# Performance work log

Measured on AMD Instinct MI355X. Metric: run time of the kernel, lower is better.

## Reference

```python
import jax, jax.numpy as jnp
import numpy as np

DIM = 192
HEADS = 6
WIN = (2, 7, 7)
N = WIN[0] * WIN[1] * WIN[2]  # 98
B_ = 2048
NW = 512


def _relative_position_index():
    d, h, w = np.meshgrid(np.arange(WIN[0]), np.arange(WIN[1]), np.arange(WIN[2]), indexing='ij')
    coords = np.stack([d.ravel(), h.ravel(), w.ravel()])  # [3, N]
    rel = coords[:, :, None] - coords[:, None, :]          # [3, N, N]
    rel = rel.transpose(1, 2, 0).astype(np.int64)
    rel[:, :, 0] += WIN[0] - 1
    rel[:, :, 1] += WIN[1] - 1
    rel[:, :, 2] += WIN[2] - 1
    rel[:, :, 0] *= (2 * WIN[1] - 1) * (2 * WIN[2] - 1)
    rel[:, :, 1] *= 2 * WIN[2] - 1
    return rel.sum(-1).astype(np.int32)  # [N, N]


def setup_inputs() -> dict:
    key = jax.random.key(0)
    ks = jax.random.split(key, 6)
    table_size = (2 * WIN[0] - 1) * (2 * WIN[1] - 1) * (2 * WIN[2] - 1)  # 507
    return {
        'x': jax.random.normal(ks[0], (B_, N, DIM), dtype=jnp.float32),
        'mask': jnp.zeros((NW, N, N), dtype=jnp.float32),
        'qkv_w': jax.random.normal(ks[1], (3 * DIM, DIM), dtype=jnp.float32) * 0.02,
        'qkv_b': jnp.zeros((3 * DIM,), dtype=jnp.float32),
        'proj_w': jax.random.normal(ks[2], (DIM, DIM), dtype=jnp.float32) * 0.02,
        'proj_b': jnp.zeros((DIM,), dtype=jnp.float32),
        'bias_table': jax.random.truncated_normal(ks[3], -2.0, 2.0, (table_size, HEADS), dtype=jnp.float32) * 0.02,
        'rel_idx': jnp.asarray(_relative_position_index()),
    }


def reference(x, mask, qkv_w, qkv_b, proj_w, proj_b, bias_table, rel_idx):
    b_, n, c = x.shape
    hd = c // HEADS
    scale = hd ** -0.5
    qkv = x @ qkv_w.T + qkv_b                      # [B_, N, 3C]
    qkv = qkv.reshape(b_, n, 3, HEADS, hd).transpose(2, 0, 3, 1, 4)
    q, k, v = qkv[0], qkv[1], qkv[2]               # each [B_, H, N, hd]
    attn = jnp.einsum('bhnd,bhmd->bhnm', q * scale, k)
    # relative position bias gather: [N*N] -> [N, N, H] -> [H, N, N]
    bias = bias_table[rel_idx.reshape(-1)].reshape(n, n, HEADS).transpose(2, 0, 1)
    attn = attn + bias[None]
    nw = mask.shape[0]
    attn = attn.reshape(b_ // nw, nw, HEADS, n, n) + mask[None, :, None]
    attn = attn.reshape(b_, HEADS, n, n)
    attn = jax.nn.softmax(attn, axis=-1)
    out = jnp.einsum('bhnm,bhmd->bhnd', attn, v)   # [B_, H, N, hd]
    out = out.transpose(0, 2, 1, 3).reshape(b_, n, c)
    return out @ proj_w.T + proj_b
```

## Files before the change

### kernel.cpp

```cpp
#include <hip/hip_runtime.h>
#include <hip/hip_bf16.h>
#include <stdint.h>

#define SEQ    98
#define DIMC   192
#define NHEADS 6
#define HDIM   32
#define NBATCH 2048
#define NWIN   512
#define SCALE  0.17677669529663687f

#define OFF_QKVW  0u
#define OFF_PROJW 221184u
#define OFF_BIAS  294912u
#define OFF_FLAGS 445440u
#define OFF_Q     447488u
#define PERWIN_E  (NHEADS * SEQ * HDIM)
#define PERWIN_B  ((size_t)PERWIN_E * 2 * 3)

typedef __attribute__((ext_vector_type(4)))  float f32x4;
typedef __attribute__((ext_vector_type(16))) float f32x16;
typedef __attribute__((ext_vector_type(8)))  short bf16x8;

static __device__ __forceinline__ uint16_t f2bf(float f) {
    uint32_t u = __builtin_bit_cast(uint32_t, f);
    u += 0x7fffu + ((u >> 16) & 1u);
    return (uint16_t)(u >> 16);
}
static __device__ __forceinline__ float bf2f(uint16_t h) {
    uint32_t u = ((uint32_t)h) << 16;
    return __builtin_bit_cast(float, u);
}

__global__ void __launch_bounds__(256) k_prep(
    const float* __restrict__ qkv_w, const float* __restrict__ proj_w,
    const float* __restrict__ bias_table, const int* __restrict__ rel_idx,
    uint16_t* __restrict__ qkv_wb, uint16_t* __restrict__ proj_wb,
    uint16_t* __restrict__ bias6b)
{
    int idx = blockIdx.x * 256 + threadIdx.x;
    if (idx < 110592) {
        qkv_wb[idx] = f2bf(qkv_w[idx]);
    } else if (idx < 147456) {
        int t = idx - 110592;
        proj_wb[t] = f2bf(proj_w[t]);
    } else {
        int t = idx - 147456;
        int h = t / (112 * 112);
        int rr = t % (112 * 112);
        int i = rr / 112, j = rr % 112;
        float v = -1e30f;
        if (i < SEQ && j < SEQ) v = bias_table[rel_idx[i * SEQ + j] * NHEADS + h];
        bias6b[t] = f2bf(v);
    }
}

__global__ void __launch_bounds__(256) k_flags(const float* __restrict__ mask,
                                               int* __restrict__ flags)
{
    int w = blockIdx.x;
    __shared__ int sf;
    if (threadIdx.x == 0) sf = 0;
    __syncthreads();
    const float* m = mask + (size_t)w * (SEQ * SEQ);
    int local = 0;
    for (int i = threadIdx.x; i < SEQ * SEQ; i += 256) local |= (m[i] != 0.0f);
    if (local) atomicOr(&sf, 1);
    __syncthreads();
    if (threadIdx.x == 0) flags[w] = sf;
}

__global__ void __launch_bounds__(256) k_qkv(
    const float* __restrict__ x, const float* __restrict__ qkv_b,
    const uint16_t* __restrict__ qkv_wb,
    uint16_t* __restrict__ q_ws, uint16_t* __restrict__ k_ws,
    uint16_t* __restrict__ v_ws, int b0)
{
    __shared__ uint16_t xs[128][200];
    const int lb = blockIdx.x, b = b0 + lb, tid = threadIdx.x;
    const int lane = tid & 63, wave = tid >> 6;
    const int l31 = lane & 31, lh = lane >> 5;

    const float4* x4 = (const float4*)(x + (size_t)b * SEQ * DIMC);
    for (int i = tid; i < SEQ * DIMC / 4; i += 256) {
        float4 v = x4[i];
        int row = i / 48, col = (i % 48) * 4;
        union { uint16_t s[4]; uint2 u; } pk;
        pk.s[0] = f2bf(v.x); pk.s[1] = f2bf(v.y);
        pk.s[2] = f2bf(v.z); pk.s[3] = f2bf(v.w);
        *(uint2*)&xs[row][col] = pk.u;
    }
    for (int i = tid; i < 30 * 100; i += 256) {
        int row = 98 + i / 100, c2 = (i % 100) * 2;
        *(uint32_t*)&xs[row][c2] = 0;
    }
    __syncthreads();

    for (int mt = 0; mt < 4; mt++) {
        bf16x8 afr[12];
        #pragma unroll
        for (int kk = 0; kk < 12; kk++)
            afr[kk] = *(const bf16x8*)&xs[mt * 32 + l31][kk * 16 + lh * 8];

        for (int ot = wave; ot < 18; ot += 4) {
            const uint16_t* wp = qkv_wb + (size_t)(ot * 32 + l31) * DIMC + lh * 8;
            bf16x8 bfr[12];
            #pragma unroll
            for (int kk = 0; kk < 12; kk++)
                bfr[kk] = *(const bf16x8*)(wp + kk * 16);
            float qb = qkv_b[ot * 32 + l31];

            f32x16 acc;
            #pragma unroll
            for (int i = 0; i < 16; i++) acc[i] = 0.0f;
            #pragma unroll
            for (int kk = 0; kk < 12; kk++)
                acc = __builtin_amdgcn_mfma_f32_32x32x16_bf16(afr[kk], bfr[kk], acc, 0, 0, 0);

            const int sec = ot / 6, head = ot % 6;
            uint16_t* outp = (sec == 0 ? q_ws : sec == 1 ? k_ws : v_ws)
                           + (size_t)(lb * NHEADS + head) * SEQ * HDIM + l31;
            #pragma unroll
            for (int r = 0; r < 16; r++) {
                int row = mt * 32 + 4 * lh + (r & 3) + 8 * (r >> 2);
                if (row < SEQ) outp[row * HDIM] = f2bf(acc[r] + qb);
            }
        }
    }
}

__global__ void __launch_bounds__(256) k_attn(
    const uint16_t* __restrict__ q_ws, const uint16_t* __restrict__ k_ws,
    const uint16_t* __restrict__ v_ws, const uint16_t* __restrict__ bias6b,
    const float* __restrict__ mask, const int* __restrict__ flags,
    const uint16_t* __restrict__ proj_wb, const float* __restrict__ proj_b,
    float* __restrict__ out, int b0)
{
    __shared__ uint16_t att_s[98][200];
    __shared__ uint16_t k_s[98][40];
    __shared__ uint16_t vT_s[32][136];
    __shared__ uint16_t p_s[4][16][40];

    const int lb = blockIdx.x, b = b0 + lb, tid = threadIdx.x;
    const int lane = tid & 63, wave = tid >> 6;
    const int l15 = lane & 15, lq = lane >> 4;
    const int useMask = flags[b & (NWIN - 1)];
    const float* maskp = mask + (size_t)(b & (NWIN - 1)) * (SEQ * SEQ);

    for (int i = tid; i < 32 * 20; i += 256) {
        int row = i / 20, c = 96 + (i % 20) * 2;
        *(uint32_t*)&vT_s[row][c] = 0;
    }

    for (int h = 0; h < NHEADS; h++) {
        if (h) __syncthreads();
        const uint32_t* kp = (const uint32_t*)(k_ws + (size_t)(lb * NHEADS + h) * SEQ * HDIM);
        const uint32_t* vp = (const uint32_t*)(v_ws + (size_t)(lb * NHEADS + h) * SEQ * HDIM);
        for (int i = tid; i < SEQ * 16; i += 256) {
            int row = i >> 4, cp = i & 15;
            uint32_t kv = kp[i];
            *(uint32_t*)&k_s[row][cp * 2] = kv;
            uint32_t vv = vp[i];
            vT_s[cp * 2][row]     = (uint16_t)(vv & 0xffff);
            vT_s[cp * 2 + 1][row] = (uint16_t)(vv >> 16);
        }
        __syncthreads();

        for (int mt = wave; mt < 7; mt += 4) {
            int qrow = mt * 16 + l15; qrow = qrow < SEQ ? qrow : SEQ - 1;
            bf16x8 aq = *(const bf16x8*)(q_ws +
                ((size_t)(lb * NHEADS + h) * SEQ + qrow) * HDIM + lq * 8);

            f32x4 sacc[7];
            #pragma unroll
            for (int jt = 0; jt < 7; jt++) {
                int krow = jt * 16 + l15; krow = krow < SEQ ? krow : SEQ - 1;
                bf16x8 bk = *(const bf16x8*)&k_s[krow][lq * 8];
                f32x4 z = {0.f, 0.f, 0.f, 0.f};
                sacc[jt] = __builtin_amdgcn_mfma_f32_16x16x32_bf16(aq, bk, z, 0, 0, 0);
            }

            float p[7][4], rowmax[4], rowsum[4];
            #pragma unroll
            for (int r = 0; r < 4; r++) rowmax[r] = -3e38f;
            #pragma unroll
            for (int jt = 0; jt < 7; jt++) {
                int j = jt * 16 + l15;
                #pragma unroll
                for (int r = 0; r < 4; r++) {
                    int i_ = mt * 16 + lq * 4 + r;
                    float s = sacc[jt][r] * SCALE +
                              bf2f(bias6b[(h * 112 + i_) * 112 + j]);
                    if (useMask && i_ < SEQ && j < SEQ) s += maskp[i_ * SEQ + j];
                    p[jt][r] = s;
                    rowmax[r] = fmaxf(rowmax[r], s);
                }
            }
            #pragma unroll
            for (int r = 0; r < 4; r++) {
                float m = rowmax[r];
                m = fmaxf(m, __shfl_xor(m, 1));
                m = fmaxf(m, __shfl_xor(m, 2));
                m = fmaxf(m, __shfl_xor(m, 4));
                m = fmaxf(m, __shfl_xor(m, 8));
                rowmax[r] = m; rowsum[r] = 0.f;
            }
            #pragma unroll
            for (int jt = 0; jt < 7; jt++)
                #pragma unroll
                for (int r = 0; r < 4; r++) {
                    float e = __expf(p[jt][r] - rowmax[r]);
                    p[jt][r] = e; rowsum[r] += e;
                }
            #pragma unroll
            for (int r = 0; r < 4; r++) {
                float s2 = rowsum[r];
                s2 += __shfl_xor(s2, 1);
                s2 += __shfl_xor(s2, 2);
                s2 += __shfl_xor(s2, 4);
                s2 += __shfl_xor(s2, 8);
                rowsum[r] = 1.0f / s2;
            }

            f32x4 oacc[2];
            oacc[0] = (f32x4){0.f,0.f,0.f,0.f};
            oacc[1] = (f32x4){0.f,0.f,0.f,0.f};
            #pragma unroll
            for (int kk = 0; kk < 4; kk++) {
                int t1 = kk * 2 + 1;
                #pragma unroll
                for (int r = 0; r < 4; r++) {
                    p_s[wave][lq * 4 + r][l15]      = f2bf(p[kk * 2][r]);
                    p_s[wave][lq * 4 + r][16 + l15] = f2bf(t1 < 7 ? p[t1][r] : 0.f);
                }
                bf16x8 ap = *(const bf16x8*)&p_s[wave][l15][lq * 8];
                #pragma unroll
                for (int o = 0; o < 2; o++) {
                    bf16x8 bv = *(const bf16x8*)&vT_s[o * 16 + l15][kk * 32 + lq * 8];
                    oacc[o] = __builtin_amdgcn_mfma_f32_16x16x32_bf16(ap, bv, oacc[o], 0, 0, 0);
                }
            }
            #pragma unroll
            for (int o = 0; o < 2; o++)
                #pragma unroll
                for (int r = 0; r < 4; r++) {
                    int row = mt * 16 + lq * 4 + r;
                    if (row < SEQ)
                        att_s[row][h * HDIM + o * 16 + l15] =
                            f2bf(oacc[o][r] * rowsum[r]);
                }
        }
    }
    __syncthreads();

    for (int ot = wave; ot < 12; ot += 4) {
        const uint16_t* wp = proj_wb + (size_t)(ot * 16 + l15) * DIMC + lq * 8;
        bf16x8 bw[6];
        #pragma unroll
        for (int kk = 0; kk < 6; kk++) bw[kk] = *(const bf16x8*)(wp + kk * 32);
        float pb = proj_b[ot * 16 + l15];
        for (int mt = 0; mt < 7; mt++) {
            int arow = mt * 16 + l15; arow = arow < SEQ ? arow : SEQ - 1;
            f32x4 pacc = {0.f, 0.f, 0.f, 0.f};
            #pragma unroll
            for (int kk = 0; kk < 6; kk++) {
                bf16x8 aa = *(const bf16x8*)&att_s[arow][kk * 32 + lq * 8];
                pacc = __builtin_amdgcn_mfma_f32_16x16x32_bf16(aa, bw[kk], pacc, 0, 0, 0);
            }
            #pragma unroll
            for (int r = 0; r < 4; r++) {
                int row = mt * 16 + lq * 4 + r;
                if (row < SEQ)
                    out[((size_t)b * SEQ + row) * DIMC + ot * 16 + l15] = pacc[r] + pb;
            }
        }
    }
}

extern "C" void kernel_launch(void* const* d_in, const int* in_sizes, int n_in,
                              void* d_out, int out_size, void* d_ws, size_t ws_size,
                              hipStream_t stream) {
    const float* x          = (const float*)d_in[0];
    const float* mask       = (const float*)d_in[1];
    const float* qkv_w      = (const float*)d_in[2];
    const float* qkv_b      = (const float*)d_in[3];
    const float* proj_w     = (const float*)d_in[4];
    const float* proj_b     = (const float*)d_in[5];
    const float* bias_table = (const float*)d_in[6];
    const int*   rel_idx    = (const int*)d_in[7];
    float* out = (float*)d_out;
    char*  ws  = (char*)d_ws;

    uint16_t* qkv_wb  = (uint16_t*)(ws + OFF_QKVW);
    uint16_t* proj_wb = (uint16_t*)(ws + OFF_PROJW);
    uint16_t* bias6b  = (uint16_t*)(ws + OFF_BIAS);
    int*      flags   = (int*)(ws + OFF_FLAGS);

    int chunk = NBATCH;
    if (ws_size < (size_t)OFF_Q + (size_t)NBATCH * PERWIN_B) {
        size_t cap = ws_size > OFF_Q ? (ws_size - OFF_Q) / PERWIN_B : 1;
        if (cap < 1) cap = 1;
        if (cap > NBATCH) cap = NBATCH;
        chunk = (int)cap;
    }
    uint16_t* q_ws = (uint16_t*)(ws + OFF_Q);
    uint16_t* k_ws = q_ws + (size_t)chunk * PERWIN_E;
    uint16_t* v_ws = k_ws + (size_t)chunk * PERWIN_E;

    k_prep<<<870, 256, 0, stream>>>(qkv_w, proj_w, bias_table, rel_idx,
                                    qkv_wb, proj_wb, bias6b);
    k_flags<<<NWIN, 256, 0, stream>>>(mask, flags);
    for (int b0 = 0; b0 < NBATCH; b0 += chunk) {
        int nb = chunk < NBATCH - b0 ? chunk : NBATCH - b0;
        k_qkv<<<nb, 256, 0, stream>>>(x, qkv_b, qkv_wb, q_ws, k_ws, v_ws, b0);
        k_attn<<<nb, 256, 0, stream>>>(q_ws, k_ws, v_ws, bias6b, mask, flags,
                                       proj_wb, proj_b, out, b0);
    }
}
```

Before: 850.0 us.

## Split attention per head, move projection to separate GEMM kernel, vectorize stores

```diff
diff --git a/kernel.cpp b/kernel.cpp
--- a/kernel.cpp
+++ b/kernel.cpp
@@ -15,11 +15,10 @@
 #define OFF_BIAS  294912u
 #define OFF_FLAGS 445440u
 #define OFF_Q     447488u
-#define PERWIN_E  (NHEADS * SEQ * HDIM)
-#define PERWIN_B  ((size_t)PERWIN_E * 2 * 3)
+#define PERWIN_E  18816
+#define PERWIN_B  ((size_t)PERWIN_E * 2 * 4)
 
 typedef __attribute__((ext_vector_type(4)))  float f32x4;
-typedef __attribute__((ext_vector_type(16))) float f32x16;
 typedef __attribute__((ext_vector_type(8)))  short bf16x8;
 
 static __device__ __forceinline__ uint16_t f2bf(float f) {
@@ -30,6 +29,11 @@
 static __device__ __forceinline__ float bf2f(uint16_t h) {
     uint32_t u = ((uint32_t)h) << 16;
     return __builtin_bit_cast(float, u);
+}
+static __device__ __forceinline__ uint32_t cvtpk(float a, float b) {
+    uint32_t d;
+    asm("v_cvt_pk_bf16_f32 %0, %1, %2" : "=v"(d) : "v"(a), "v"(b));
+    return d;
 }
 
 __global__ void __launch_bounds__(256) k_prep(
@@ -70,209 +74,211 @@
     if (threadIdx.x == 0) flags[w] = sf;
 }
 
-__global__ void __launch_bounds__(256) k_qkv(
+__global__ void __launch_bounds__(256, 4) k_qkv(
     const float* __restrict__ x, const float* __restrict__ qkv_b,
     const uint16_t* __restrict__ qkv_wb,
     uint16_t* __restrict__ q_ws, uint16_t* __restrict__ k_ws,
     uint16_t* __restrict__ v_ws, int b0)
 {
-    __shared__ uint16_t xs[128][200];
+    __shared__ uint16_t xs[112][200];
+    __shared__ uint16_t obuf[4][16][40];
     const int lb = blockIdx.x, b = b0 + lb, tid = threadIdx.x;
     const int lane = tid & 63, wave = tid >> 6;
-    const int l31 = lane & 31, lh = lane >> 5;
+    const int l15 = lane & 15, lq = lane >> 4;
 
     const float4* x4 = (const float4*)(x + (size_t)b * SEQ * DIMC);
     for (int i = tid; i < SEQ * DIMC / 4; i += 256) {
         float4 v = x4[i];
         int row = i / 48, col = (i % 48) * 4;
-        union { uint16_t s[4]; uint2 u; } pk;
-        pk.s[0] = f2bf(v.x); pk.s[1] = f2bf(v.y);
-        pk.s[2] = f2bf(v.z); pk.s[3] = f2bf(v.w);
-        *(uint2*)&xs[row][col] = pk.u;
-    }
-    for (int i = tid; i < 30 * 100; i += 256) {
-        int row = 98 + i / 100, c2 = (i % 100) * 2;
-        *(uint32_t*)&xs[row][c2] = 0;
-    }
-    __syncthreads();
-
-    for (int mt = 0; mt < 4; mt++) {
-        bf16x8 afr[12];
-        #pragma unroll
-        for (int kk = 0; kk < 12; kk++)
-            afr[kk] = *(const bf16x8*)&xs[mt * 32 + l31][kk * 16 + lh * 8];
-
-        for (int ot = wave; ot < 18; ot += 4) {
-            const uint16_t* wp = qkv_wb + (size_t)(ot * 32 + l31) * DIMC + lh * 8;
-            bf16x8 bfr[12];
-            #pragma unroll
-            for (int kk = 0; kk < 12; kk++)
-                bfr[kk] = *(const bf16x8*)(wp + kk * 16);
-            float qb = qkv_b[ot * 32 + l31];
-
-            f32x16 acc;
-            #pragma unroll
-            for (int i = 0; i < 16; i++) acc[i] = 0.0f;
-            #pragma unroll
-            for (int kk = 0; kk < 12; kk++)
-                acc = __builtin_amdgcn_mfma_f32_32x32x16_bf16(afr[kk], bfr[kk], acc, 0, 0, 0);
-
-            const int sec = ot / 6, head = ot % 6;
-            uint16_t* outp = (sec == 0 ? q_ws : sec == 1 ? k_ws : v_ws)
-                           + (size_t)(lb * NHEADS + head) * SEQ * HDIM + l31;
-            #pragma unroll
-            for (int r = 0; r < 16; r++) {
-                int row = mt * 32 + 4 * lh + (r & 3) + 8 * (r >> 2);
-                if (row < SEQ) outp[row * HDIM] = f2bf(acc[r] + qb);
-            }
-        }
-    }
-}
-
-__global__ void __launch_bounds__(256) k_attn(
+        uint2 pk;
+        pk.x = cvtpk(v.x, v.y);
+        pk.y = cvtpk(v.z, v.w);
+        *(uint2*)&xs[row][col] = pk;
+    }
+    __syncthreads();
+
+    for (int ot = wave; ot < 18; ot += 4) {
+        bf16x8 bfr[2][6];
+        float qb[2];
+        #pragma unroll
+        for (int o = 0; o < 2; o++) {
+            const uint16_t* wp = qkv_wb + (size_t)(ot * 32 + o * 16 + l15) * DIMC + lq * 8;
+            #pragma unroll
+            for (int kk = 0; kk < 6; kk++) bfr[o][kk] = *(const bf16x8*)(wp + kk * 32);
+            qb[o] = qkv_b[ot * 32 + o * 16 + l15];
+        }
+        const int sec = ot / 6, head = ot % 6;
+        uint16_t* outp = (sec == 0 ? q_ws : sec == 1 ? k_ws : v_ws)
+                       + (size_t)(lb * NHEADS + head) * (SEQ * HDIM);
+        for (int mt = 0; mt < 7; mt++) {
+            bf16x8 afr[6];
+            #pragma unroll
+            for (int kk = 0; kk < 6; kk++)
+                afr[kk] = *(const bf16x8*)&xs[mt * 16 + l15][kk * 32 + lq * 8];
+            f32x4 a0 = {0.f,0.f,0.f,0.f}, a1 = {0.f,0.f,0.f,0.f};
+            #pragma unroll
+            for (int kk = 0; kk < 6; kk++) {
+                a0 = __builtin_amdgcn_mfma_f32_16x16x32_bf16(afr[kk], bfr[0][kk], a0, 0, 0, 0);
+                a1 = __builtin_amdgcn_mfma_f32_16x16x32_bf16(afr[kk], bfr[1][kk], a1, 0, 0, 0);
+            }
+            #pragma unroll
+            for (int r = 0; r < 4; r++) {
+                obuf[wave][lq * 4 + r][l15]      = f2bf(a0[r] + qb[0]);
+                obuf[wave][lq * 4 + r][16 + l15] = f2bf(a1[r] + qb[1]);
+            }
+            int r16 = lane >> 2, m8 = (lane & 3) * 8;
+            int token = mt * 16 + r16;
+            bf16x8 ov = *(const bf16x8*)&obuf[wave][r16][m8];
+            if (token < SEQ)
+                *(bf16x8*)(outp + token * HDIM + m8) = ov;
+        }
+    }
+}
+
+__global__ void __launch_bounds__(256, 4) k_attn(
     const uint16_t* __restrict__ q_ws, const uint16_t* __restrict__ k_ws,
     const uint16_t* __restrict__ v_ws, const uint16_t* __restrict__ bias6b,
     const float* __restrict__ mask, const int* __restrict__ flags,
-    const uint16_t* __restrict__ proj_wb, const float* __restrict__ proj_b,
-    float* __restrict__ out, int b0)
-{
-    __shared__ uint16_t att_s[98][200];
+    uint16_t* __restrict__ att, int b0)
+{
     __shared__ uint16_t k_s[98][40];
     __shared__ uint16_t vT_s[32][136];
-    __shared__ uint16_t p_s[4][16][40];
-
-    const int lb = blockIdx.x, b = b0 + lb, tid = threadIdx.x;
+    __shared__ uint16_t ps[4][16][40];
+
+    const int bid = blockIdx.x;
+    const int lb = bid / 6, h = bid % 6;
+    const int bg = b0 + lb;
+    const int tid = threadIdx.x, lane = tid & 63, wave = tid >> 6;
+    const int l15 = lane & 15, lq = lane >> 4;
+    const int useMask = flags[bg & (NWIN - 1)];
+    const float* maskp = mask + (size_t)(bg & (NWIN - 1)) * (SEQ * SEQ);
+
+    for (int i = tid; i < 32 * 19; i += 256) {
+        int d = i / 19, c = 98 + (i % 19) * 2;
+        *(uint32_t*)&vT_s[d][c] = 0;
+    }
+    const uint32_t* kp = (const uint32_t*)(k_ws + (size_t)(lb * NHEADS + h) * (SEQ * HDIM));
+    const uint32_t* vp = (const uint32_t*)(v_ws + (size_t)(lb * NHEADS + h) * (SEQ * HDIM));
+    for (int i = tid; i < SEQ * 16; i += 256) {
+        int row = i >> 4, cp = i & 15;
+        uint32_t kv = kp[i];
+        *(uint32_t*)&k_s[row][cp * 2] = kv;
+        uint32_t vv = vp[i];
+        vT_s[cp * 2][row]     = (uint16_t)(vv & 0xffff);
+        vT_s[cp * 2 + 1][row] = (uint16_t)(vv >> 16);
+    }
+    __syncthreads();
+
+    const uint16_t* qbase = q_ws + (size_t)(lb * NHEADS + h) * (SEQ * HDIM);
+    for (int mt = wave; mt < 7; mt += 4) {
+        int qrow = mt * 16 + l15; if (qrow > 97) qrow = 97;
+        bf16x8 aq = *(const bf16x8*)(qbase + qrow * HDIM + lq * 8);
+
+        float p[7][4], rowmax[4], rowsum[4];
+        #pragma unroll
+        for (int r = 0; r < 4; r++) rowmax[r] = -3e38f;
+        #pragma unroll
+        for (int jt = 0; jt < 7; jt++) {
+            int krow = jt * 16 + l15; if (krow > 97) krow = 97;
+            bf16x8 bk = *(const bf16x8*)&k_s[krow][lq * 8];
+            f32x4 z = {0.f,0.f,0.f,0.f};
+            f32x4 s4 = __builtin_amdgcn_mfma_f32_16x16x32_bf16(aq, bk, z, 0, 0, 0);
+            int j = jt * 16 + l15;
+            #pragma unroll
+            for (int r = 0; r < 4; r++) {
+                int i_ = mt * 16 + lq * 4 + r;
+                float s = s4[r] * SCALE + bf2f(bias6b[(h * 112 + i_) * 112 + j]);
+                if (useMask && i_ < SEQ && j < SEQ) s += maskp[i_ * SEQ + j];
+                p[jt][r] = s;
+                rowmax[r] = fmaxf(rowmax[r], s);
+            }
+        }
+        #pragma unroll
+        for (int r = 0; r < 4; r++) {
+            float m = rowmax[r];
+            m = fmaxf(m, __shfl_xor(m, 1));
+            m = fmaxf(m, __shfl_xor(m, 2));
+            m = fmaxf(m, __shfl_xor(m, 4));
+            m = fmaxf(m, __shfl_xor(m, 8));
+            rowmax[r] = m; rowsum[r] = 0.f;
+        }
+        #pragma unroll
+        for (int jt = 0; jt < 7; jt++)
+            #pragma unroll
+            for (int r = 0; r < 4; r++) {
+                float e = __expf(p[jt][r] - rowmax[r]);
+                p[jt][r] = e; rowsum[r] += e;
+            }
+        #pragma unroll
+        for (int r = 0; r < 4; r++) {
+            float s2 = rowsum[r];
+            s2 += __shfl_xor(s2, 1); s2 += __shfl_xor(s2, 2);
+            s2 += __shfl_xor(s2, 4); s2 += __shfl_xor(s2, 8);
+            rowsum[r] = 1.0f / s2;
+        }
+
+        f32x4 o0 = {0.f,0.f,0.f,0.f}, o1 = {0.f,0.f,0.f,0.f};
+        #pragma unroll
+        for (int kk = 0; kk < 4; kk++) {
+            #pragma unroll
+            for (int r = 0; r < 4; r++) {
+                ps[wave][lq * 4 + r][l15]      = f2bf(p[2 * kk][r]);
+                ps[wave][lq * 4 + r][16 + l15] = f2bf(2 * kk + 1 < 7 ? p[2 * kk + 1][r] : 0.f);
+            }
+            bf16x8 ap  = *(const bf16x8*)&ps[wave][l15][lq * 8];
+            bf16x8 bv0 = *(const bf16x8*)&vT_s[l15][kk * 32 + lq * 8];
+            bf16x8 bv1 = *(const bf16x8*)&vT_s[16 + l15][kk * 32 + lq * 8];
+            o0 = __builtin_amdgcn_mfma_f32_16x16x32_bf16(ap, bv0, o0, 0, 0, 0);
+            o1 = __builtin_amdgcn_mfma_f32_16x16x32_bf16(ap, bv1, o1, 0, 0, 0);
+        }
+        #pragma unroll
+        for (int r = 0; r < 4; r++) {
+            ps[wave][lq * 4 + r][l15]      = f2bf(o0[r] * rowsum[r]);
+            ps[wave][lq * 4 + r][16 + l15] = f2bf(o1[r] * rowsum[r]);
+        }
+        int r16 = lane >> 2, m8 = (lane & 3) * 8;
+        int token = mt * 16 + r16;
+        bf16x8 ov = *(const bf16x8*)&ps[wave][r16][m8];
+        if (token < SEQ)
+            *(bf16x8*)(att + ((size_t)lb * SEQ + token) * DIMC + h * HDIM + m8) = ov;
+    }
+}
+
+__global__ void __launch_bounds__(256, 4) k_proj(
+    const uint16_t* __restrict__ att, const uint16_t* __restrict__ proj_wb,
+    const float* __restrict__ proj_b, float* __restrict__ out, int M)
+{
+    __shared__ uint16_t as_[64][200];
+    const int blk = blockIdx.x, tid = threadIdx.x;
     const int lane = tid & 63, wave = tid >> 6;
     const int l15 = lane & 15, lq = lane >> 4;
-    const int useMask = flags[b & (NWIN - 1)];
-    const float* maskp = mask + (size_t)(b & (NWIN - 1)) * (SEQ * SEQ);
-
-    for (int i = tid; i < 32 * 20; i += 256) {
-        int row = i / 20, c = 96 + (i % 20) * 2;
-        *(uint32_t*)&vT_s[row][c] = 0;
-    }
-
-    for (int h = 0; h < NHEADS; h++) {
-        if (h) __syncthreads();
-        const uint32_t* kp = (const uint32_t*)(k_ws + (size_t)(lb * NHEADS + h) * SEQ * HDIM);
-        const uint32_t* vp = (const uint32_t*)(v_ws + (size_t)(lb * NHEADS + h) * SEQ * HDIM);
-        for (int i = tid; i < SEQ * 16; i += 256) {
-            int row = i >> 4, cp = i & 15;
-            uint32_t kv = kp[i];
-            *(uint32_t*)&k_s[row][cp * 2] = kv;
-            uint32_t vv = vp[i];
-            vT_s[cp * 2][row]     = (uint16_t)(vv & 0xffff);
-            vT_s[cp * 2 + 1][row] = (uint16_t)(vv >> 16);
-        }
-        __syncthreads();
-
-        for (int mt = wave; mt < 7; mt += 4) {
-            int qrow = mt * 16 + l15; qrow = qrow < SEQ ? qrow : SEQ - 1;
-            bf16x8 aq = *(const bf16x8*)(q_ws +
-                ((size_t)(lb * NHEADS + h) * SEQ + qrow) * HDIM + lq * 8);
-
-            f32x4 sacc[7];
-            #pragma unroll
-            for (int jt = 0; jt < 7; jt++) {
-                int krow = jt * 16 + l15; krow = krow < SEQ ? krow : SEQ - 1;
-                bf16x8 bk = *(const bf16x8*)&k_s[krow][lq * 8];
-                f32x4 z = {0.f, 0.f, 0.f, 0.f};
-                sacc[jt] = __builtin_amdgcn_mfma_f32_16x16x32_bf16(aq, bk, z, 0, 0, 0);
-            }
-
-            float p[7][4], rowmax[4], rowsum[4];
-            #pragma unroll
-            for (int r = 0; r < 4; r++) rowmax[r] = -3e38f;
-            #pragma unroll
-            for (int jt = 0; jt < 7; jt++) {
-                int j = jt * 16 + l15;
-                #pragma unroll
-                for (int r = 0; r < 4; r++) {
-                    int i_ = mt * 16 + lq * 4 + r;
-                    float s = sacc[jt][r] * SCALE +
-                              bf2f(bias6b[(h * 112 + i_) * 112 + j]);
-                    if (useMask && i_ < SEQ && j < SEQ) s += maskp[i_ * SEQ + j];
-                    p[jt][r] = s;
-                    rowmax[r] = fmaxf(rowmax[r], s);
-                }
-            }
-            #pragma unroll
-            for (int r = 0; r < 4; r++) {
-                float m = rowmax[r];
-                m = fmaxf(m, __shfl_xor(m, 1));
-                m = fmaxf(m, __shfl_xor(m, 2));
-                m = fmaxf(m, __shfl_xor(m, 4));
-                m = fmaxf(m, __shfl_xor(m, 8));
-                rowmax[r] = m; rowsum[r] = 0.f;
-            }
-            #pragma unroll
-            for (int jt = 0; jt < 7; jt++)
-                #pragma unroll
-                for (int r = 0; r < 4; r++) {
-                    float e = __expf(p[jt][r] - rowmax[r]);
-                    p[jt][r] = e; rowsum[r] += e;
-                }
-            #pragma unroll
-            for (int r = 0; r < 4; r++) {
-                float s2 = rowsum[r];
-                s2 += __shfl_xor(s2, 1);
-                s2 += __shfl_xor(s2, 2);
-                s2 += __shfl_xor(s2, 4);
-                s2 += __shfl_xor(s2, 8);
-                rowsum[r] = 1.0f / s2;
-            }
-
-            f32x4 oacc[2];
-            oacc[0] = (f32x4){0.f,0.f,0.f,0.f};
-            oacc[1] = (f32x4){0.f,0.f,0.f,0.f};
-            #pragma unroll
-            for (int kk = 0; kk < 4; kk++) {
-                int t1 = kk * 2 + 1;
-                #pragma unroll
-                for (int r = 0; r < 4; r++) {
-                    p_s[wave][lq * 4 + r][l15]      = f2bf(p[kk * 2][r]);
-                    p_s[wave][lq * 4 + r][16 + l15] = f2bf(t1 < 7 ? p[t1][r] : 0.f);
-                }
-                bf16x8 ap = *(const bf16x8*)&p_s[wave][l15][lq * 8];
-                #pragma unroll
-                for (int o = 0; o < 2; o++) {
-                    bf16x8 bv = *(const bf16x8*)&vT_s[o * 16 + l15][kk * 32 + lq * 8];
-                    oacc[o] = __builtin_amdgcn_mfma_f32_16x16x32_bf16(ap, bv, oacc[o], 0, 0, 0);
-                }
-            }
-            #pragma unroll
-            for (int o = 0; o < 2; o++)
-                #pragma unroll
-                for (int r = 0; r < 4; r++) {
-                    int row = mt * 16 + lq * 4 + r;
-                    if (row < SEQ)
-                        att_s[row][h * HDIM + o * 16 + l15] =
-                            f2bf(oacc[o][r] * rowsum[r]);
-                }
-        }
-    }
-    __syncthreads();
-
-    for (int ot = wave; ot < 12; ot += 4) {
+
+    for (int i = tid; i < 64 * DIMC / 8; i += 256) {
+        int el = i * 8;
+        int lr = el / DIMC, c = el % DIMC;
+        int gr = blk * 64 + lr; if (gr >= M) gr = M - 1;
+        *(bf16x8*)&as_[lr][c] = *(const bf16x8*)(att + (size_t)gr * DIMC + c);
+    }
+    __syncthreads();
+
+    bf16x8 a[6];
+    #pragma unroll
+    for (int kk = 0; kk < 6; kk++)
+        a[kk] = *(const bf16x8*)&as_[wave * 16 + l15][kk * 32 + lq * 8];
+
+    for (int ot = 0; ot < 12; ot++) {
         const uint16_t* wp = proj_wb + (size_t)(ot * 16 + l15) * DIMC + lq * 8;
-        bf16x8 bw[6];
-        #pragma unroll
-        for (int kk = 0; kk < 6; kk++) bw[kk] = *(const bf16x8*)(wp + kk * 32);
+        f32x4 acc = {0.f,0.f,0.f,0.f};
+        #pragma unroll
+        for (int kk = 0; kk < 6; kk++) {
+            bf16x8 bw = *(const bf16x8*)(wp + kk * 32);
+            acc = __builtin_amdgcn_mfma_f32_16x16x32_bf16(a[kk], bw, acc, 0, 0, 0);
+        }
         float pb = proj_b[ot * 16 + l15];
-        for (int mt = 0; mt < 7; mt++) {
-            int arow = mt * 16 + l15; arow = arow < SEQ ? arow : SEQ - 1;
-            f32x4 pacc = {0.f, 0.f, 0.f, 0.f};
-            #pragma unroll
-            for (int kk = 0; kk < 6; kk++) {
-                bf16x8 aa = *(const bf16x8*)&att_s[arow][kk * 32 + lq * 8];
-                pacc = __builtin_amdgcn_mfma_f32_16x16x32_bf16(aa, bw[kk], pacc, 0, 0, 0);
-            }
-            #pragma unroll
-            for (int r = 0; r < 4; r++) {
-                int row = mt * 16 + lq * 4 + r;
-                if (row < SEQ)
-                    out[((size_t)b * SEQ + row) * DIMC + ot * 16 + l15] = pacc[r] + pb;
-            }
+        #pragma unroll
+        for (int r = 0; r < 4; r++) {
+            int gr = blk * 64 + wave * 16 + lq * 4 + r;
+            if (gr < M) out[(size_t)gr * DIMC + ot * 16 + l15] = acc[r] + pb;
         }
     }
 }
@@ -303,9 +309,10 @@
         if (cap > NBATCH) cap = NBATCH;
         chunk = (int)cap;
     }
-    uint16_t* q_ws = (uint16_t*)(ws + OFF_Q);
-    uint16_t* k_ws = q_ws + (size_t)chunk * PERWIN_E;
-    uint16_t* v_ws = k_ws + (size_t)chunk * PERWIN_E;
+    uint16_t* q_ws   = (uint16_t*)(ws + OFF_Q);
+    uint16_t* k_ws   = q_ws + (size_t)chunk * PERWIN_E;
+    uint16_t* v_ws   = k_ws + (size_t)chunk * PERWIN_E;
+    uint16_t* att_ws = v_ws + (size_t)chunk * PERWIN_E;
 
     k_prep<<<870, 256, 0, stream>>>(qkv_w, proj_w, bias_table, rel_idx,
                                     qkv_wb, proj_wb, bias6b);
@@ -313,7 +320,10 @@
     for (int b0 = 0; b0 < NBATCH; b0 += chunk) {
         int nb = chunk < NBATCH - b0 ? chunk : NBATCH - b0;
         k_qkv<<<nb, 256, 0, stream>>>(x, qkv_b, qkv_wb, q_ws, k_ws, v_ws, b0);
-        k_attn<<<nb, 256, 0, stream>>>(q_ws, k_ws, v_ws, bias6b, mask, flags,
-                                       proj_wb, proj_b, out, b0);
-    }
-}
+        k_attn<<<nb * NHEADS, 256, 0, stream>>>(q_ws, k_ws, v_ws, bias6b, mask,
+                                                flags, att_ws, b0);
+        int M = nb * SEQ;
+        k_proj<<<(M + 63) / 64, 256, 0, stream>>>(att_ws, proj_wb, proj_b,
+                                                  out + (size_t)b0 * SEQ * DIMC, M);
+    }
+}
```

After: 716.2 us. -15.7%, faster.
